# Optimization experiments

Hardware: AMD Instinct MI355X
Metric: run time of the kernel (lower is better)

Reference implementation:

```python
import jax, jax.numpy as jnp
import numpy as np

BETA = 0.9      # LIF leak
THRESH = 1.0    # snntorch Leaky default threshold
SLOPE = 25.0    # fast_sigmoid surrogate slope

@jax.custom_vjp
def spike(x):
    # Heaviside forward, fast_sigmoid surrogate backward
    return (x > 0).astype(x.dtype)

def _spike_fwd(x):
    return spike(x), x

def _spike_bwd(x, g):
    return (g / (SLOPE * jnp.abs(x) + 1.0) ** 2,)

spike.defvjp(_spike_fwd, _spike_bwd)


def setup_inputs() -> dict:
    key = jax.random.key(0)
    k0, k1, k2, k3, k4 = jax.random.split(key, 5)
    B, T, I, H, C = 256, 100, 512, 1024, 8
    x = jax.random.normal(k0, (B, T, I), dtype=jnp.float32)
    s1 = 1.0 / np.sqrt(I)
    s2 = 1.0 / np.sqrt(H)
    W1 = jax.random.uniform(k1, (H, I), jnp.float32, -s1, s1)
    b1 = jax.random.uniform(k2, (H,), jnp.float32, -s1, s1)
    W2 = jax.random.uniform(k3, (C, H), jnp.float32, -s2, s2)
    b2 = jax.random.uniform(k4, (C,), jnp.float32, -s2, s2)
    return {"x": x, "W1": W1, "b1": b1, "W2": W2, "b2": b2}


def reference(x, W1, b1, W2, b2):
    # x: [B, T, I]
    B, T, I = x.shape
    H = W1.shape[0]
    # fc1 for all timesteps as one big GEMM (same math as per-step loop).
    cur = jnp.einsum('bti,hi->tbh', x, W1) + b1  # [T, B, H]

    def step(mem, c):
        # snntorch Leaky (reset_mechanism='subtract'):
        reset = spike(mem - THRESH)
        mem_new = BETA * mem + c - reset * THRESH
        spk = spike(mem_new - THRESH)
        return mem_new, spk

    mem0 = jnp.zeros((B, H), dtype=x.dtype)
    _, spk_rec = jax.lax.scan(step, mem0, cur)  # spk_rec: [T, B, H]

    # sum_t (spk_t @ W2.T + b2) == (sum_t spk_t) @ W2.T + T*b2
    spk_sum = spk_rec.sum(axis=0)  # [B, H]
    logits = spk_sum @ W2.T + T * b2  # [B, C]
    return logits
```

## Files before the change

kernel.cpp:

```cpp
#include <hip/hip_runtime.h>


#define B_   256
#define T_   100
#define I_   512
#define H_   1024
#define C_   8
#define M_   (B_ * T_)
#define KS_  1024
#define SC   64.0f
#define ISC  (1.0f / 4096.0f)
#define CP   132

typedef _Float16 half8 __attribute__((ext_vector_type(8)));
typedef float floatx4 __attribute__((ext_vector_type(4)));

__device__ __forceinline__ void ld_g2l(const _Float16* g, _Float16* l) {
    __builtin_amdgcn_global_load_lds(
        (const __attribute__((address_space(1))) void*)g,
        (__attribute__((address_space(3))) void*)l, 16, 0, 0);
}

__global__ void __launch_bounds__(256)
split_all(const float* __restrict__ x, const float* __restrict__ W1,
          const float* __restrict__ b2, _Float16* __restrict__ Asp,
          float* __restrict__ out) {
    int g = blockIdx.x * 256 + threadIdx.x;
    if (g < B_ * C_) out[g] = 100.0f * b2[g & (C_ - 1)];
    int row = g >> 6;
    int i0 = (g & 63) * 8;
    const float* src = (row < M_) ? (x + (size_t)row * I_ + i0)
                                  : (W1 + (size_t)(row - M_) * I_ + i0);
    float4 v0 = *(const float4*)(src);
    float4 v1 = *(const float4*)(src + 4);
    float vv[8] = {v0.x, v0.y, v0.z, v0.w, v1.x, v1.y, v1.z, v1.w};
    half8 hi, lo;
#pragma unroll
    for (int j = 0; j < 8; ++j) {
        float s = vv[j] * SC;
        _Float16 h = (_Float16)s;
        hi[j] = h;
        lo[j] = (_Float16)(s - (float)h);
    }
    _Float16* r = Asp + (size_t)row * KS_ + i0;
    *(half8*)(r) = hi;
    *(half8*)(r + 512) = lo;
}

__global__ void __launch_bounds__(256, 4)
snn_mfma(const _Float16* __restrict__ Asp, const _Float16* __restrict__ Wsp,
         const float* __restrict__ b1, const float* __restrict__ W2,
         float* __restrict__ logits) {
    __shared__ union {
        struct { __align__(16) _Float16 A[128 * 64]; __align__(16) _Float16 Bm[128 * 64]; } g;
        float Cs[64 * CP];
    } sm;
    const int tid = threadIdx.x;
    const int lane = tid & 63;
    const int w = tid >> 6;

    const int xcd = blockIdx.x & 7;
    const int jj = blockIdx.x >> 3;
    const int b  = xcd * 32 + (jj >> 3);
    const int n0 = (jj & 7) * 128;

    const int wm = (w >> 1) * 64;
    const int wn = (w & 1) * 64;
    const int srow = lane >> 3;
    const int sc16 = (lane & 7) ^ srow;

    const _Float16* ag[4];
    const _Float16* bg[4];
    _Float16* al[4];
    _Float16* bl[4];
#pragma unroll
    for (int j = 0; j < 4; ++j) {
        const int r = w * 32 + j * 8 + srow;
        ag[j] = Asp + ((size_t)b * T_ + r) * KS_ + sc16 * 8;
        bg[j] = Wsp + (size_t)(n0 + r) * KS_ + sc16 * 8;
        al[j] = &sm.g.A[(w * 32 + j * 8) * 64];
        bl[j] = &sm.g.Bm[(w * 32 + j * 8) * 64];
    }

    floatx4 acc[4][4];
#pragma unroll
    for (int i = 0; i < 4; ++i)
#pragma unroll
        for (int q = 0; q < 4; ++q) acc[i][q] = (floatx4){0.f, 0.f, 0.f, 0.f};

    const int quad = lane >> 4;
    const int l15 = lane & 15;
    const int l7 = lane & 7;

    for (int kt = 0; kt < 24; ++kt) {
        const int koA = ((kt & 16) ? 512 : 0) + (kt & 7) * 64;
        const int koB = ((kt & 8)  ? 512 : 0) + (kt & 7) * 64;
        __syncthreads();
#pragma unroll
        for (int j = 0; j < 4; ++j) {
            if (j < 2 || w < 3) ld_g2l(ag[j] + koA, al[j]);
            ld_g2l(bg[j] + koB, bl[j]);
        }
        __syncthreads();
#pragma unroll
        for (int ks = 0; ks < 2; ++ks) {
            const int c16 = (ks * 4 + quad) ^ l7;
            half8 av[3], bv[4];
#pragma unroll
            for (int f = 0; f < 3; ++f)
                av[f] = *(const half8*)&sm.g.A[(wm + f * 16 + l15) * 64 + c16 * 8];
#pragma unroll
            for (int f = 0; f < 4; ++f)
                bv[f] = *(const half8*)&sm.g.Bm[(wn + f * 16 + l15) * 64 + c16 * 8];
#pragma unroll
            for (int fr = 0; fr < 3; ++fr)
#pragma unroll
                for (int fn = 0; fn < 4; ++fn)
                    acc[fr][fn] = __builtin_amdgcn_mfma_f32_16x16x32_f16(
                        av[fr], bv[fn], acc[fr][fn], 0, 0, 0);
            if (wm == 0) {
                half8 a3 = *(const half8*)&sm.g.A[(48 + l15) * 64 + c16 * 8];
#pragma unroll
                for (int fn = 0; fn < 4; ++fn)
                    acc[3][fn] = __builtin_amdgcn_mfma_f32_16x16x32_f16(
                        a3, bv[fn], acc[3][fn], 0, 0, 0);
            }
        }
    }

    float b1c[4];
#pragma unroll
    for (int fn = 0; fn < 4; ++fn) b1c[fn] = b1[n0 + wn + fn * 16 + l15];

    float mem = 0.f, ss = 0.f;
    const int myh = tid & 127;

    __syncthreads();
    if (w < 2) {
#pragma unroll
        for (int fr = 0; fr < 4; ++fr)
#pragma unroll
            for (int r = 0; r < 4; ++r) {
                float* dst = &sm.Cs[(fr * 16 + quad * 4 + r) * CP + wn + l15];
#pragma unroll
                for (int fn = 0; fn < 4; ++fn)
                    dst[fn * 16] = acc[fr][fn][r] * ISC + b1c[fn];
            }
    }
    __syncthreads();
    if (tid < 128) {
#pragma unroll 8
        for (int t = 0; t < 64; ++t) {
            float c = sm.Cs[t * CP + myh];
            float reset = (mem > 1.0f) ? 1.0f : 0.0f;
            mem = 0.9f * mem + c - reset;
            ss += (mem > 1.0f) ? 1.0f : 0.0f;
        }
    }
    __syncthreads();
    if (w >= 2) {
#pragma unroll
        for (int fr = 0; fr < 3; ++fr)
#pragma unroll
            for (int r = 0; r < 4; ++r) {
                float* dst = &sm.Cs[(fr * 16 + quad * 4 + r) * CP + wn + l15];
#pragma unroll
                for (int fn = 0; fn < 4; ++fn)
                    dst[fn * 16] = acc[fr][fn][r] * ISC + b1c[fn];
            }
    }
    __syncthreads();
    if (tid < 128) {
#pragma unroll 6
        for (int t = 0; t < 36; ++t) {
            float c = sm.Cs[t * CP + myh];
            float reset = (mem > 1.0f) ? 1.0f : 0.0f;
            mem = 0.9f * mem + c - reset;
            ss += (mem > 1.0f) ? 1.0f : 0.0f;
        }
#pragma unroll
        for (int c = 0; c < C_; ++c) {
            float v = ss * W2[c * H_ + n0 + myh];
#pragma unroll
            for (int off = 32; off; off >>= 1) v += __shfl_down(v, off, 64);
            if (lane == 0) atomicAdd(&logits[b * C_ + c], v);
        }
    }
}

extern "C" void kernel_launch(void* const* d_in, const int* in_sizes, int n_in,
                              void* d_out, int out_size, void* d_ws, size_t ws_size,
                              hipStream_t stream) {
    const float* x  = (const float*)d_in[0];
    const float* W1 = (const float*)d_in[1];
    const float* b1 = (const float*)d_in[2];
    const float* W2 = (const float*)d_in[3];
    const float* b2 = (const float*)d_in[4];
    float* out = (float*)d_out;

    char* ws = (char*)d_ws;
    _Float16* Asp = (_Float16*)ws;
    _Float16* Wsp = (_Float16*)(ws + (size_t)M_ * KS_ * 2);

    hipLaunchKernelGGL(split_all, dim3((M_ + H_) * 64 / 256), dim3(256), 0, stream,
                       x, W1, b2, Asp, out);
    hipLaunchKernelGGL(snn_mfma, dim3(B_ * 8), dim3(256), 0, stream,
                       Asp, Wsp, b1, W2, out);
}
```

Before: 195.2 us.

## Recompute A high half from fp32 x in GEMM; store only low half

The split kernel now writes only the fp16 low residual of x, and the GEMM kernel reads fp32 x straight from global memory into registers and converts it to the high half on the fly. B (W1 hi/lo) stays staged in LDS, while the A operands bypass LDS. This removes the hi-half write and re-read of A and halves A's LDS staging. In exchange it adds uncoalesced per-lane global loads of fp32 x (twice the bytes of fp16) inside the K loop, plus conversion work. Rounding also changes from round-to-nearest to round-toward-zero (cvt_pkrtz).

```diff
diff --git a/kernel.cpp b/kernel.cpp
--- a/kernel.cpp
+++ b/kernel.cpp
@@ -7,12 +7,13 @@
 #define H_   1024
 #define C_   8
 #define M_   (B_ * T_)
-#define KS_  1024
 #define SC   64.0f
 #define ISC  (1.0f / 4096.0f)
 #define CP   132
+#define APAD 128
 
 typedef _Float16 half8 __attribute__((ext_vector_type(8)));
+typedef __fp16 fp16x2 __attribute__((ext_vector_type(2)));
 typedef float floatx4 __attribute__((ext_vector_type(4)));
 
 __device__ __forceinline__ void ld_g2l(const _Float16* g, _Float16* l) {
@@ -21,38 +22,61 @@
         (__attribute__((address_space(3))) void*)l, 16, 0, 0);
 }
 
+__device__ __forceinline__ half8 pk_hi(float4 f0, float4 f1) {
+    fp16x2 p0 = __builtin_amdgcn_cvt_pkrtz(f0.x * SC, f0.y * SC);
+    fp16x2 p1 = __builtin_amdgcn_cvt_pkrtz(f0.z * SC, f0.w * SC);
+    fp16x2 p2 = __builtin_amdgcn_cvt_pkrtz(f1.x * SC, f1.y * SC);
+    fp16x2 p3 = __builtin_amdgcn_cvt_pkrtz(f1.z * SC, f1.w * SC);
+    half8 h;
+    h[0] = (_Float16)p0[0]; h[1] = (_Float16)p0[1];
+    h[2] = (_Float16)p1[0]; h[3] = (_Float16)p1[1];
+    h[4] = (_Float16)p2[0]; h[5] = (_Float16)p2[1];
+    h[6] = (_Float16)p3[0]; h[7] = (_Float16)p3[1];
+    return h;
+}
+
 __global__ void __launch_bounds__(256)
-split_all(const float* __restrict__ x, const float* __restrict__ W1,
-          const float* __restrict__ b2, _Float16* __restrict__ Asp,
-          float* __restrict__ out) {
+split_lo_w(const float* __restrict__ x, const float* __restrict__ W1,
+           const float* __restrict__ b2, _Float16* __restrict__ Alo,
+           _Float16* __restrict__ Wsp, float* __restrict__ out) {
     int g = blockIdx.x * 256 + threadIdx.x;
     if (g < B_ * C_) out[g] = 100.0f * b2[g & (C_ - 1)];
     int row = g >> 6;
     int i0 = (g & 63) * 8;
-    const float* src = (row < M_) ? (x + (size_t)row * I_ + i0)
-                                  : (W1 + (size_t)(row - M_) * I_ + i0);
-    float4 v0 = *(const float4*)(src);
-    float4 v1 = *(const float4*)(src + 4);
-    float vv[8] = {v0.x, v0.y, v0.z, v0.w, v1.x, v1.y, v1.z, v1.w};
-    half8 hi, lo;
-#pragma unroll
-    for (int j = 0; j < 8; ++j) {
-        float s = vv[j] * SC;
-        _Float16 h = (_Float16)s;
-        hi[j] = h;
-        lo[j] = (_Float16)(s - (float)h);
-    }
-    _Float16* r = Asp + (size_t)row * KS_ + i0;
-    *(half8*)(r) = hi;
-    *(half8*)(r + 512) = lo;
+    if (row < M_) {
+        const float* src = x + (size_t)row * I_ + i0;
+        float4 v0 = *(const float4*)(src);
+        float4 v1 = *(const float4*)(src + 4);
+        float vv[8] = {v0.x, v0.y, v0.z, v0.w, v1.x, v1.y, v1.z, v1.w};
+        half8 hi = pk_hi(v0, v1);
+        half8 lo;
+#pragma unroll
+        for (int j = 0; j < 8; ++j)
+            lo[j] = (_Float16)(vv[j] * SC - (float)hi[j]);
+        *(half8*)(Alo + (size_t)row * I_ + i0) = lo;
+    } else {
+        int h = row - M_;
+        const float* src = W1 + (size_t)h * I_ + i0;
+        float4 v0 = *(const float4*)(src);
+        float4 v1 = *(const float4*)(src + 4);
+        float vv[8] = {v0.x, v0.y, v0.z, v0.w, v1.x, v1.y, v1.z, v1.w};
+        half8 hi = pk_hi(v0, v1);
+        half8 lo;
+#pragma unroll
+        for (int j = 0; j < 8; ++j)
+            lo[j] = (_Float16)(vv[j] * SC - (float)hi[j]);
+        _Float16* r = Wsp + (size_t)h * 1024 + i0;
+        *(half8*)(r) = hi;
+        *(half8*)(r + 512) = lo;
+    }
 }
 
 __global__ void __launch_bounds__(256, 4)
-snn_mfma(const _Float16* __restrict__ Asp, const _Float16* __restrict__ Wsp,
-         const float* __restrict__ b1, const float* __restrict__ W2,
-         float* __restrict__ logits) {
+snn_mfma(const float* __restrict__ x, const _Float16* __restrict__ Alo,
+         const _Float16* __restrict__ Wsp, const float* __restrict__ b1,
+         const float* __restrict__ W2, float* __restrict__ logits) {
     __shared__ union {
-        struct { __align__(16) _Float16 A[128 * 64]; __align__(16) _Float16 Bm[128 * 64]; } g;
+        struct { __align__(16) _Float16 Bh[128 * 64]; __align__(16) _Float16 Bl[128 * 64]; } g;
         float Cs[64 * CP];
     } sm;
     const int tid = threadIdx.x;
@@ -69,61 +93,75 @@
     const int srow = lane >> 3;
     const int sc16 = (lane & 7) ^ srow;
 
-    const _Float16* ag[4];
-    const _Float16* bg[4];
-    _Float16* al[4];
-    _Float16* bl[4];
-#pragma unroll
-    for (int j = 0; j < 4; ++j) {
-        const int r = w * 32 + j * 8 + srow;
-        ag[j] = Asp + ((size_t)b * T_ + r) * KS_ + sc16 * 8;
-        bg[j] = Wsp + (size_t)(n0 + r) * KS_ + sc16 * 8;
-        al[j] = &sm.g.A[(w * 32 + j * 8) * 64];
-        bl[j] = &sm.g.Bm[(w * 32 + j * 8) * 64];
-    }
-
-    floatx4 acc[4][4];
-#pragma unroll
-    for (int i = 0; i < 4; ++i)
-#pragma unroll
-        for (int q = 0; q < 4; ++q) acc[i][q] = (floatx4){0.f, 0.f, 0.f, 0.f};
-
     const int quad = lane >> 4;
     const int l15 = lane & 15;
     const int l7 = lane & 7;
 
-    for (int kt = 0; kt < 24; ++kt) {
-        const int koA = ((kt & 16) ? 512 : 0) + (kt & 7) * 64;
-        const int koB = ((kt & 8)  ? 512 : 0) + (kt & 7) * 64;
+    const _Float16* bg[4];
+    _Float16* blh[4];
+    _Float16* bll[4];
+#pragma unroll
+    for (int j = 0; j < 4; ++j) {
+        const int r = w * 32 + j * 8 + srow;
+        bg[j]  = Wsp + (size_t)(n0 + r) * 1024 + sc16 * 8;
+        blh[j] = &sm.g.Bh[(w * 32 + j * 8) * 64];
+        bll[j] = &sm.g.Bl[(w * 32 + j * 8) * 64];
+    }
+
+    const float* xrow[4];
+    const _Float16* lrow[4];
+#pragma unroll
+    for (int fr = 0; fr < 4; ++fr) {
+        int r = b * T_ + wm + fr * 16 + l15;
+        int rc = (r < M_) ? r : (M_ - 1);
+        xrow[fr] = x + (size_t)rc * I_;
+        lrow[fr] = Alo + (size_t)r * I_;
+    }
+
+    floatx4 acc[4][4];
+#pragma unroll
+    for (int i = 0; i < 4; ++i)
+#pragma unroll
+        for (int q = 0; q < 4; ++q) acc[i][q] = (floatx4){0.f, 0.f, 0.f, 0.f};
+
+    for (int kt = 0; kt < 8; ++kt) {
+        const int ko = kt * 64;
         __syncthreads();
 #pragma unroll
         for (int j = 0; j < 4; ++j) {
-            if (j < 2 || w < 3) ld_g2l(ag[j] + koA, al[j]);
-            ld_g2l(bg[j] + koB, bl[j]);
+            ld_g2l(bg[j] + ko, blh[j]);
+            ld_g2l(bg[j] + 512 + ko, bll[j]);
         }
         __syncthreads();
 #pragma unroll
         for (int ks = 0; ks < 2; ++ks) {
-            const int c16 = (ks * 4 + quad) ^ l7;
-            half8 av[3], bv[4];
-#pragma unroll
-            for (int f = 0; f < 3; ++f)
-                av[f] = *(const half8*)&sm.g.A[(wm + f * 16 + l15) * 64 + c16 * 8];
-#pragma unroll
-            for (int f = 0; f < 4; ++f)
-                bv[f] = *(const half8*)&sm.g.Bm[(wn + f * 16 + l15) * 64 + c16 * 8];
-#pragma unroll
-            for (int fr = 0; fr < 3; ++fr)
-#pragma unroll
-                for (int fn = 0; fn < 4; ++fn)
-                    acc[fr][fn] = __builtin_amdgcn_mfma_f32_16x16x32_f16(
-                        av[fr], bv[fn], acc[fr][fn], 0, 0, 0);
-            if (wm == 0) {
-                half8 a3 = *(const half8*)&sm.g.A[(48 + l15) * 64 + c16 * 8];
-#pragma unroll
-                for (int fn = 0; fn < 4; ++fn)
-                    acc[3][fn] = __builtin_amdgcn_mfma_f32_16x16x32_f16(
-                        a3, bv[fn], acc[3][fn], 0, 0, 0);
+            const int kbase = ko + ks * 32 + quad * 8;
+            half8 avh[4], avl[4];
+#pragma unroll
+            for (int fr = 0; fr < 4; ++fr) {
+                if (fr < 3 || wm == 0) {
+                    float4 f0 = *(const float4*)(xrow[fr] + kbase);
+                    float4 f1 = *(const float4*)(xrow[fr] + kbase + 4);
+                    avh[fr] = pk_hi(f0, f1);
+                    avl[fr] = *(const half8*)(lrow[fr] + kbase);
+                }
+            }
+#pragma unroll
+            for (int fn = 0; fn < 4; ++fn) {
+                const int phys = ((ks * 4 + quad) ^ l7) * 8;
+                half8 bvh = *(const half8*)&sm.g.Bh[(wn + fn * 16 + l15) * 64 + phys];
+                half8 bvl = *(const half8*)&sm.g.Bl[(wn + fn * 16 + l15) * 64 + phys];
+#pragma unroll
+                for (int fr = 0; fr < 4; ++fr) {
+                    if (fr < 3 || wm == 0) {
+                        acc[fr][fn] = __builtin_amdgcn_mfma_f32_16x16x32_f16(
+                            avh[fr], bvh, acc[fr][fn], 0, 0, 0);
+                        acc[fr][fn] = __builtin_amdgcn_mfma_f32_16x16x32_f16(
+                            avl[fr], bvh, acc[fr][fn], 0, 0, 0);
+                        acc[fr][fn] = __builtin_amdgcn_mfma_f32_16x16x32_f16(
+                            avh[fr], bvl, acc[fr][fn], 0, 0, 0);
+                    }
+                }
             }
         }
     }
@@ -199,11 +237,11 @@
     float* out = (float*)d_out;
 
     char* ws = (char*)d_ws;
-    _Float16* Asp = (_Float16*)ws;
-    _Float16* Wsp = (_Float16*)(ws + (size_t)M_ * KS_ * 2);
-
-    hipLaunchKernelGGL(split_all, dim3((M_ + H_) * 64 / 256), dim3(256), 0, stream,
-                       x, W1, b2, Asp, out);
+    _Float16* Alo = (_Float16*)ws;
+    _Float16* Wsp = Alo + (size_t)(M_ + APAD) * I_;
+
+    hipLaunchKernelGGL(split_lo_w, dim3((M_ + H_) * 64 / 256), dim3(256), 0, stream,
+                       x, W1, b2, Alo, Wsp, out);
     hipLaunchKernelGGL(snn_mfma, dim3(B_ * 8), dim3(256), 0, stream,
-                       Asp, Wsp, b1, W2, out);
-}
+                       x, Alo, Wsp, b1, W2, out);
+}
```

Result: slower. 345.3 us (+76.9%).
